# Kernel tuning notes

Hardware: AMD Instinct MI355X
Metric: run time of the kernel (lower is better)

## Reference

```python
import jax, jax.numpy as jnp
import numpy as np

WEIGHT = 0.1
TEMPERATURE = 0.07
EPS_NORM = 1e-12   # F.normalize eps
EPS_DEN = 1e-6     # denominator eps in pos_mask.sum()


def setup_inputs() -> dict:
    key = jax.random.key(0)
    k1, k2 = jax.random.split(key)
    features = jax.random.normal(k1, (4, 1000, 2048), dtype=jnp.float32)
    target = jax.random.randint(k2, (4, 1000), 0, 16, dtype=jnp.int64)
    return {"features": features, "target": target}


def _per_sample_loss(f, t):
    # f: [N, C], t: [N]
    N = f.shape[0]
    # F.normalize(dim=1)
    norm = jnp.maximum(jnp.linalg.norm(f, axis=1, keepdims=True), EPS_NORM)
    f = f / norm
    # [N, N] cosine similarities scaled by temperature
    sim = jnp.matmul(f, f.T) / TEMPERATURE
    eye = jnp.eye(N, dtype=f.dtype)
    pos = (t[:, None] == t[None, :]).astype(f.dtype) * (1.0 - eye)
    neg = 1.0 - pos - eye
    pos_sim = sim * pos
    # -log(exp(pos_sim) / (exp(pos_sim) + sum_j exp(sim)*neg))  summed over ALL entries
    denom = jnp.exp(pos_sim) + jnp.sum(jnp.exp(sim) * neg, axis=1, keepdims=True)
    loss_mat = jnp.log(denom) - pos_sim
    pos_sum = pos.sum()
    return loss_mat.sum() / (pos_sum + EPS_DEN), pos_sum


def reference(features, target):
    # features: [B, N, C] (already 3-D: no subsampling / interpolation paths fire)
    losses, pos_sums = jax.vmap(_per_sample_loss)(features, target)
    valid = pos_sums > 0
    num_pairs = valid.sum().astype(features.dtype)
    total = jnp.where(valid, losses, 0.0).sum()
    return jnp.where(num_pairs > 0, WEIGHT * total / num_pairs,
                     jnp.asarray(WEIGHT * 0.1, dtype=features.dtype))
```

## Files before the change

### kernel.cpp

```cpp
#include <hip/hip_runtime.h>
#include <math.h>

#define BB 4
#define NN 1000
#define NP 1024
#define CC 2048
#define TINV (1.0f / 0.07f)

#define FNORM_BYTES ((size_t)BB * NP * CC * 2)
#define SIMP_BYTES  ((size_t)2 * BB * NP * NP * 4)
#define RL_BYTES    ((size_t)BB * NP * 4)

typedef __bf16 bf16x8 __attribute__((ext_vector_type(8)));
typedef float  f32x4  __attribute__((ext_vector_type(4)));

__device__ __forceinline__ void load_lds16(const void* g, void* l) {
    __builtin_amdgcn_global_load_lds(
        (const __attribute__((address_space(1))) unsigned int*)g,
        (__attribute__((address_space(3))) unsigned int*)l, 16, 0, 0);
}

__device__ __forceinline__ float blk_sum(float v, volatile float* lds) {
    int lane = threadIdx.x & 63;
    int wid  = threadIdx.x >> 6;
#pragma unroll
    for (int off = 32; off; off >>= 1) v += __shfl_down(v, off);
    __syncthreads();
    if (lane == 0) lds[wid] = v;
    __syncthreads();
    return lds[0] + lds[1] + lds[2] + lds[3];
}

__device__ __forceinline__ float wave_sum(float v) {
#pragma unroll
    for (int off = 32; off; off >>= 1) v += __shfl_down(v, off);
    return __shfl(v, 0);
}

__global__ __launch_bounds__(256) void norm_bf16_kernel(const float* __restrict__ f,
                                                        __bf16* __restrict__ out) {
    __shared__ float lds[4];
    __shared__ float scale_s;
    const int blk = blockIdx.x;
    const int b = blk >> 10, r = blk & (NP - 1);
    __bf16* dst = out + ((size_t)b * NP + r) * CC;
    const int tid = threadIdx.x;

    if (r >= NN) {
        ((uint4*)dst)[tid] = make_uint4(0u, 0u, 0u, 0u);
        return;
    }
    const float* src = f + ((size_t)b * NN + r) * CC;

    float ss = 0.f;
#pragma unroll
    for (int h = 0; h < 2; ++h) {
        float4 v = ((const float4*)src)[tid + h * 256];
        ss += v.x * v.x + v.y * v.y + v.z * v.z + v.w * v.w;
    }
    float tot = blk_sum(ss, lds);
    if (tid == 0) scale_s = 1.0f / fmaxf(sqrtf(tot), 1e-12f);
    __syncthreads();
    const float sc = scale_s;

    float4 v0 = ((const float4*)src)[tid * 2];
    float4 v1 = ((const float4*)src)[tid * 2 + 1];
    bf16x8 o;
    o[0] = (__bf16)(v0.x * sc); o[1] = (__bf16)(v0.y * sc);
    o[2] = (__bf16)(v0.z * sc); o[3] = (__bf16)(v0.w * sc);
    o[4] = (__bf16)(v1.x * sc); o[5] = (__bf16)(v1.y * sc);
    o[6] = (__bf16)(v1.z * sc); o[7] = (__bf16)(v1.w * sc);
    *(bf16x8*)(dst + tid * 8) = o;
}

__global__ __launch_bounds__(512) void simgemm_mfma(const __bf16* __restrict__ fn,
                                                    float* __restrict__ simp) {
    __shared__ __bf16 As[128 * 32];
    __shared__ __bf16 Bs[128 * 32];

    const int bz = blockIdx.z;
    const int b  = bz >> 1;
    const int kbeg = (bz & 1) * (CC / 2);
    const int tI = blockIdx.y * 128;
    const int tJ = blockIdx.x * 128;
    const __bf16* base = fn + (size_t)b * NP * CC;
    float* S = simp + (size_t)bz * NP * NP;

    const int tid  = threadIdx.x;
    const int wid  = tid >> 6;
    const int lane = tid & 63;
    const int wm   = wid >> 2;
    const int wn   = wid & 3;
    const int q    = lane >> 4;
    const int ln   = lane & 15;

    const int srow  = wid * 16 + (lane >> 2);
    const int selem = (lane & 3) * 8;
    const __bf16* gA = base + (size_t)(tI + srow) * CC + kbeg + selem;
    const __bf16* gB = base + (size_t)(tJ + srow) * CC + kbeg + selem;
    __bf16* lA = As + wid * 512;
    __bf16* lB = Bs + wid * 512;

    f32x4 acc[4][2] = {};

    for (int k0 = 0; k0 < CC / 2; k0 += 32) {
        load_lds16(gA + k0, lA);
        load_lds16(gB + k0, lB);
        __syncthreads();

        bf16x8 af[4], bf[2];
#pragma unroll
        for (int mt = 0; mt < 4; ++mt)
            af[mt] = *(const bf16x8*)&As[(wm * 64 + mt * 16 + ln) * 32 + q * 8];
#pragma unroll
        for (int nt = 0; nt < 2; ++nt)
            bf[nt] = *(const bf16x8*)&Bs[(wn * 32 + nt * 16 + ln) * 32 + q * 8];
#pragma unroll
        for (int mt = 0; mt < 4; ++mt)
#pragma unroll
            for (int nt = 0; nt < 2; ++nt)
                acc[mt][nt] = __builtin_amdgcn_mfma_f32_16x16x32_bf16(
                    af[mt], bf[nt], acc[mt][nt], 0, 0, 0);
        __syncthreads();
    }

#pragma unroll
    for (int mt = 0; mt < 4; ++mt) {
#pragma unroll
        for (int nt = 0; nt < 2; ++nt) {
            const int col = tJ + wn * 32 + nt * 16 + ln;
#pragma unroll
            for (int r = 0; r < 4; ++r) {
                const int row = tI + wm * 64 + mt * 16 + q * 4 + r;
                S[(size_t)row * NP + col] = acc[mt][nt][r] * TINV;
            }
        }
    }
}

__global__ __launch_bounds__(256) void rowloss_kernel(const float* __restrict__ simp,
                                                      const int* __restrict__ tgt,
                                                      float* __restrict__ rloss,
                                                      float* __restrict__ rpos) {
    __shared__ int ts[NN];
    const int b = blockIdx.y;
    const int wid = threadIdx.x >> 6, lane = threadIdx.x & 63;
    const int* t = tgt + (size_t)b * NN;
    for (int j = threadIdx.x; j < NN; j += 256) ts[j] = t[j];
    __syncthreads();

    const int i = blockIdx.x * 4 + wid;
    const float* r0 = simp + (size_t)(2 * b) * NP * NP + (size_t)i * NP;
    const float* r1 = r0 + (size_t)NP * NP;
    const int ti = ts[i];

    float sneg = 0.f, pcnt = 0.f;
    for (int g = lane; g < NN / 4; g += 64) {
        float4 a = ((const float4*)r0)[g];
        float4 c = ((const float4*)r1)[g];
        float4 v = make_float4(a.x + c.x, a.y + c.y, a.z + c.z, a.w + c.w);
        int4 tj = *(const int4*)&ts[g * 4];
        const int j = g * 4;
        if (j + 0 != i) { if (tj.x == ti) pcnt += 1.f; else sneg += __expf(v.x); }
        if (j + 1 != i) { if (tj.y == ti) pcnt += 1.f; else sneg += __expf(v.y); }
        if (j + 2 != i) { if (tj.z == ti) pcnt += 1.f; else sneg += __expf(v.z); }
        if (j + 3 != i) { if (tj.w == ti) pcnt += 1.f; else sneg += __expf(v.w); }
    }
    const float Sv = wave_sum(sneg);
    const float p  = wave_sum(pcnt);

    float term = 0.f;
    for (int g = lane; g < NN / 4; g += 64) {
        float4 a = ((const float4*)r0)[g];
        float4 c = ((const float4*)r1)[g];
        float4 v = make_float4(a.x + c.x, a.y + c.y, a.z + c.z, a.w + c.w);
        int4 tj = *(const int4*)&ts[g * 4];
        const int j = g * 4;
        if (j + 0 != i && tj.x == ti) term += __logf(__expf(v.x) + Sv) - v.x;
        if (j + 1 != i && tj.y == ti) term += __logf(__expf(v.y) + Sv) - v.y;
        if (j + 2 != i && tj.z == ti) term += __logf(__expf(v.z) + Sv) - v.z;
        if (j + 3 != i && tj.w == ti) term += __logf(__expf(v.w) + Sv) - v.w;
    }
    const float tt = wave_sum(term);
    if (lane == 0) {
        rloss[b * NP + i] = tt + ((float)NN - p) * __logf(1.f + Sv);
        rpos [b * NP + i] = p;
    }
}

__global__ __launch_bounds__(256) void final_kernel(const float* __restrict__ rloss,
                                                    const float* __restrict__ rpos,
                                                    float* __restrict__ out) {
    __shared__ float lds[4];
    float total = 0.f, np = 0.f;
    for (int b = 0; b < BB; ++b) {
        float l = 0.f, p = 0.f;
        for (int i = threadIdx.x; i < NN; i += 256) {
            l += rloss[b * NP + i];
            p += rpos [b * NP + i];
        }
        float ls = blk_sum(l, lds);
        float ps = blk_sum(p, lds);
        if (ps > 0.f) { total += ls / (ps + 1e-6f); np += 1.f; }
    }
    if (threadIdx.x == 0)
        out[0] = (np > 0.f) ? 0.1f * total / np : 0.1f * 0.1f;
}

extern "C" void kernel_launch(void* const* d_in, const int* in_sizes, int n_in,
                              void* d_out, int out_size, void* d_ws, size_t ws_size,
                              hipStream_t stream) {
    const float* feat = (const float*)d_in[0];
    const int*   tgt  = (const int*)d_in[1];
    __bf16* fnorm = (__bf16*)d_ws;
    float*  simp  = (float*)((char*)d_ws + FNORM_BYTES);
    float*  rloss = (float*)((char*)d_ws + FNORM_BYTES + SIMP_BYTES);
    float*  rpos  = (float*)((char*)d_ws + FNORM_BYTES + SIMP_BYTES + RL_BYTES);

    norm_bf16_kernel<<<dim3(BB * NP), 256, 0, stream>>>(feat, fnorm);
    simgemm_mfma<<<dim3(NP / 128, NP / 128, 2 * BB), 512, 0, stream>>>(fnorm, simp);
    rowloss_kernel<<<dim3(NN / 4, BB), 256, 0, stream>>>(simp, tgt, rloss, rpos);
    final_kernel<<<1, 256, 0, stream>>>(rloss, rpos, (float*)d_out);
}
```

Before: 123.6 us.

## Restructure similarity GEMM to 32x32 MFMA with BK=64 swizzled LDS, cache rows

The GEMM kernel moves from 512 threads using 16x16x32 MFMA with BK=32 to 256 threads, each wave computing a 64x64 sub-tile with 32x32x16 MFMA, a BK=64 K-step and an XOR-swizzled LDS layout. This gives more reuse per LDS fragment, fewer barriers per unit of K, and fewer bank conflicts. Separately, the row-loss kernel keeps the summed similarity row in LDS so the second pass no longer re-reads both partial rows from global memory. The cost is more accumulator registers per thread and more LDS per block, which may reduce occupancy.

```diff
diff --git a/kernel.cpp b/kernel.cpp
--- a/kernel.cpp
+++ b/kernel.cpp
@@ -6,6 +6,7 @@
 #define NP 1024
 #define CC 2048
 #define TINV (1.0f / 0.07f)
+#define BK 64
 
 #define FNORM_BYTES ((size_t)BB * NP * CC * 2)
 #define SIMP_BYTES  ((size_t)2 * BB * NP * NP * 4)
@@ -13,6 +14,7 @@
 
 typedef __bf16 bf16x8 __attribute__((ext_vector_type(8)));
 typedef float  f32x4  __attribute__((ext_vector_type(4)));
+typedef float  f32x16 __attribute__((ext_vector_type(16)));
 
 __device__ __forceinline__ void load_lds16(const void* g, void* l) {
     __builtin_amdgcn_global_load_lds(
@@ -73,10 +75,10 @@
     *(bf16x8*)(dst + tid * 8) = o;
 }
 
-__global__ __launch_bounds__(512) void simgemm_mfma(const __bf16* __restrict__ fn,
+__global__ __launch_bounds__(256) void simgemm_mfma(const __bf16* __restrict__ fn,
                                                     float* __restrict__ simp) {
-    __shared__ __bf16 As[128 * 32];
-    __shared__ __bf16 Bs[128 * 32];
+    __shared__ __bf16 As[128 * BK];
+    __shared__ __bf16 Bs[128 * BK];
 
     const int bz = blockIdx.z;
     const int b  = bz >> 1;
@@ -89,50 +91,55 @@
     const int tid  = threadIdx.x;
     const int wid  = tid >> 6;
     const int lane = tid & 63;
-    const int wm   = wid >> 2;
-    const int wn   = wid & 3;
-    const int q    = lane >> 4;
-    const int ln   = lane & 15;
-
-    const int srow  = wid * 16 + (lane >> 2);
-    const int selem = (lane & 3) * 8;
-    const __bf16* gA = base + (size_t)(tI + srow) * CC + kbeg + selem;
-    const __bf16* gB = base + (size_t)(tJ + srow) * CC + kbeg + selem;
-    __bf16* lA = As + wid * 512;
-    __bf16* lB = Bs + wid * 512;
-
-    f32x4 acc[4][2] = {};
-
-    for (int k0 = 0; k0 < CC / 2; k0 += 32) {
-        load_lds16(gA + k0, lA);
-        load_lds16(gB + k0, lB);
+    const int wm   = wid >> 1;
+    const int wn   = wid & 1;
+    const int ln32 = lane & 31;
+    const int kh   = lane >> 5;
+    const int sw   = ln32 & 7;
+
+    const int srow   = tid >> 3;
+    const int schunk = (tid & 7) ^ (srow & 7);
+    const __bf16* gA = base + (size_t)(tI + srow) * CC + kbeg + schunk * 8;
+    const __bf16* gB = base + (size_t)(tJ + srow) * CC + kbeg + schunk * 8;
+    __bf16* lA = As + (size_t)wid * 8 * BK;
+    __bf16* lB = Bs + (size_t)wid * 8 * BK;
+
+    f32x16 acc[2][2] = {};
+
+    for (int k0 = 0; k0 < CC / 2; k0 += BK) {
+#pragma unroll
+        for (int r = 0; r < 4; ++r)
+            load_lds16(gA + k0 + (size_t)r * 32 * CC, lA + r * 32 * BK);
+#pragma unroll
+        for (int r = 0; r < 4; ++r)
+            load_lds16(gB + k0 + (size_t)r * 32 * CC, lB + r * 32 * BK);
         __syncthreads();
 
-        bf16x8 af[4], bf[2];
-#pragma unroll
-        for (int mt = 0; mt < 4; ++mt)
-            af[mt] = *(const bf16x8*)&As[(wm * 64 + mt * 16 + ln) * 32 + q * 8];
-#pragma unroll
-        for (int nt = 0; nt < 2; ++nt)
-            bf[nt] = *(const bf16x8*)&Bs[(wn * 32 + nt * 16 + ln) * 32 + q * 8];
-#pragma unroll
-        for (int mt = 0; mt < 4; ++mt)
-#pragma unroll
-            for (int nt = 0; nt < 2; ++nt)
-                acc[mt][nt] = __builtin_amdgcn_mfma_f32_16x16x32_bf16(
-                    af[mt], bf[nt], acc[mt][nt], 0, 0, 0);
+#pragma unroll
+        for (int kc = 0; kc < 4; ++kc) {
+            const int c = kc * 2 + kh;
+            const int co = (c ^ sw) * 8;
+            bf16x8 a0 = *(const bf16x8*)&As[(wm * 64      + ln32) * BK + co];
+            bf16x8 a1 = *(const bf16x8*)&As[(wm * 64 + 32 + ln32) * BK + co];
+            bf16x8 b0 = *(const bf16x8*)&Bs[(wn * 64      + ln32) * BK + co];
+            bf16x8 b1 = *(const bf16x8*)&Bs[(wn * 64 + 32 + ln32) * BK + co];
+            acc[0][0] = __builtin_amdgcn_mfma_f32_32x32x16_bf16(a0, b0, acc[0][0], 0, 0, 0);
+            acc[0][1] = __builtin_amdgcn_mfma_f32_32x32x16_bf16(a0, b1, acc[0][1], 0, 0, 0);
+            acc[1][0] = __builtin_amdgcn_mfma_f32_32x32x16_bf16(a1, b0, acc[1][0], 0, 0, 0);
+            acc[1][1] = __builtin_amdgcn_mfma_f32_32x32x16_bf16(a1, b1, acc[1][1], 0, 0, 0);
+        }
         __syncthreads();
     }
 
 #pragma unroll
-    for (int mt = 0; mt < 4; ++mt) {
-#pragma unroll
-        for (int nt = 0; nt < 2; ++nt) {
-            const int col = tJ + wn * 32 + nt * 16 + ln;
-#pragma unroll
-            for (int r = 0; r < 4; ++r) {
-                const int row = tI + wm * 64 + mt * 16 + q * 4 + r;
-                S[(size_t)row * NP + col] = acc[mt][nt][r] * TINV;
+    for (int at = 0; at < 2; ++at) {
+#pragma unroll
+        for (int bt = 0; bt < 2; ++bt) {
+            const int col = tJ + wn * 64 + bt * 32 + ln32;
+#pragma unroll
+            for (int r = 0; r < 16; ++r) {
+                const int row = tI + wm * 64 + at * 32 + (r & 3) + 8 * (r >> 2) + 4 * kh;
+                S[(size_t)row * NP + col] = acc[at][bt][r] * TINV;
             }
         }
     }
@@ -143,6 +150,7 @@
                                                       float* __restrict__ rloss,
                                                       float* __restrict__ rpos) {
     __shared__ int ts[NN];
+    __shared__ float rowv[4][NP];
     const int b = blockIdx.y;
     const int wid = threadIdx.x >> 6, lane = threadIdx.x & 63;
     const int* t = tgt + (size_t)b * NN;
@@ -159,6 +167,7 @@
         float4 a = ((const float4*)r0)[g];
         float4 c = ((const float4*)r1)[g];
         float4 v = make_float4(a.x + c.x, a.y + c.y, a.z + c.z, a.w + c.w);
+        *(float4*)&rowv[wid][g * 4] = v;
         int4 tj = *(const int4*)&ts[g * 4];
         const int j = g * 4;
         if (j + 0 != i) { if (tj.x == ti) pcnt += 1.f; else sneg += __expf(v.x); }
@@ -171,9 +180,7 @@
 
     float term = 0.f;
     for (int g = lane; g < NN / 4; g += 64) {
-        float4 a = ((const float4*)r0)[g];
-        float4 c = ((const float4*)r1)[g];
-        float4 v = make_float4(a.x + c.x, a.y + c.y, a.z + c.z, a.w + c.w);
+        float4 v = *(const float4*)&rowv[wid][g * 4];
         int4 tj = *(const int4*)&ts[g * 4];
         const int j = g * 4;
         if (j + 0 != i && tj.x == ti) term += __logf(__expf(v.x) + Sv) - v.x;
@@ -218,7 +225,7 @@
     float*  rpos  = (float*)((char*)d_ws + FNORM_BYTES + SIMP_BYTES + RL_BYTES);
 
     norm_bf16_kernel<<<dim3(BB * NP), 256, 0, stream>>>(feat, fnorm);
-    simgemm_mfma<<<dim3(NP / 128, NP / 128, 2 * BB), 512, 0, stream>>>(fnorm, simp);
+    simgemm_mfma<<<dim3(NP / 128, NP / 128, 2 * BB), 256, 0, stream>>>(fnorm, simp);
     rowloss_kernel<<<dim3(NN / 4, BB), 256, 0, stream>>>(simp, tgt, rloss, rpos);
     final_kernel<<<1, 256, 0, stream>>>(rloss, rpos, (float*)d_out);
 }
```

Measured after the change: 120.5 us. 1.03x faster.
